# Kernel optimization log

Measured on AMD Instinct MI355X. Metric: run time of the kernel, lower is better.

The kernel has to match this reference:

```python
import jax, jax.numpy as jnp
import numpy as np

M, B, T, C, H, HS = 2, 8, 1024, 512, 8, 64
EPS = 1e-5

NAMES = ['x','sa_kw1','sa_kb1','sa_kw2','sa_qw1','sa_qb1','sa_qw2','sa_vw1','sa_vb1','sa_vw2',
         'sa_pw1','sa_pb1','sa_pw2','sa_pb2','ff_w1','ff_b1','ff_w2','ff_b2',
         'ln1_g','ln1_b','ln2_g','ln2_b','lnc_g','lnc_b',
         'ca_qw','ca_kvw','ca_pw1','ca_pb1','ca_pw2','ca_pb2']


def setup_inputs() -> dict:
    key = jax.random.key(0)
    it = iter(jax.random.split(key, 40))
    def w(shape, s=0.02):
        return jax.random.normal(next(it), shape, jnp.float32) * s
    d = {}
    d['x'] = jax.random.normal(next(it), (M, B, T, C), jnp.float32)
    # self-attention heads: Linear(C,HS//2)+bias -> tanh -> Linear(HS//2,HS) no bias, stacked over (M,H)
    for nm in ('k', 'q', 'v'):
        d['sa_%sw1' % nm] = w((M, H, C, HS // 2))
        d['sa_%sb1' % nm] = jnp.zeros((M, H, HS // 2), jnp.float32)
        d['sa_%sw2' % nm] = w((M, H, HS // 2, HS))
    # MHA output proj: Linear(H*HS,C//2)->tanh->Linear(C//2,C)
    d['sa_pw1'] = w((M, H * HS, C // 2)); d['sa_pb1'] = jnp.zeros((M, C // 2), jnp.float32)
    d['sa_pw2'] = w((M, C // 2, C));      d['sa_pb2'] = jnp.zeros((M, C), jnp.float32)
    # feed-forward
    d['ff_w1'] = w((M, C, 4 * C)); d['ff_b1'] = jnp.zeros((M, 4 * C), jnp.float32)
    d['ff_w2'] = w((M, 4 * C, C)); d['ff_b2'] = jnp.zeros((M, C), jnp.float32)
    # layernorms
    for nm in ('ln1', 'ln2', 'lnc'):
        d[nm + '_g'] = jnp.ones((M, C), jnp.float32)
        d[nm + '_b'] = jnp.zeros((M, C), jnp.float32)
    # cross-attention: per head q proj (no bias), per-kv-modality kv proj (no bias, 2*HS)
    d['ca_qw'] = w((M, H, C, HS))
    d['ca_kvw'] = w((M, H, M - 1, C, 2 * HS))
    d['ca_pw1'] = w((M, H * HS, C // 2)); d['ca_pb1'] = jnp.zeros((M, C // 2), jnp.float32)
    d['ca_pw2'] = w((M, C // 2, C));      d['ca_pb2'] = jnp.zeros((M, C), jnp.float32)
    return d


def _ln(x, g, b):
    mu = x.mean(-1, keepdims=True)
    var = ((x - mu) ** 2).mean(-1, keepdims=True)
    return (x - mu) * jax.lax.rsqrt(var + EPS) * g + b


def _attend(q, k, v, mask):
    # q,k,v: (B,H,T,HS); causal masked softmax attention
    aff = jnp.einsum('bhtd,bhsd->bhts', q, k) * (HS ** -0.5)
    aff = jnp.where(mask, aff, -jnp.inf)
    return jnp.einsum('bhts,bhsd->bhtd', jax.nn.softmax(aff, axis=-1), v)


def _merge(o):
    # (B,H,T,HS) -> (B,T,H*HS), matching torch.cat over heads
    return o.transpose(0, 2, 1, 3).reshape(o.shape[0], o.shape[2], -1)


def _forward(p):
    mask = jnp.tril(jnp.ones((T, T), bool))
    x = p['x']
    attended = []
    for i in range(M):  # fixed small modality loop
        xi = x[i]
        h = _ln(xi, p['ln1_g'][i], p['ln1_b'][i])
        def hm(w1, b1, w2):
            # batched over heads: Linear->tanh->Linear
            z = jnp.tanh(jnp.einsum('btc,hce->bhte', h, w1) + b1[:, None, :])
            return jnp.einsum('bhte,hed->bhtd', z, w2)
        o = _attend(hm(p['sa_qw1'][i], p['sa_qb1'][i], p['sa_qw2'][i]),
                    hm(p['sa_kw1'][i], p['sa_kb1'][i], p['sa_kw2'][i]),
                    hm(p['sa_vw1'][i], p['sa_vb1'][i], p['sa_vw2'][i]), mask)
        o = jnp.tanh(_merge(o) @ p['sa_pw1'][i] + p['sa_pb1'][i]) @ p['sa_pw2'][i] + p['sa_pb2'][i]
        xi = xi + o
        h2 = _ln(xi, p['ln2_g'][i], p['ln2_b'][i])
        xi = xi + (jax.nn.relu(h2 @ p['ff_w1'][i] + p['ff_b1'][i]) @ p['ff_w2'][i] + p['ff_b2'][i])
        attended.append(xi)
    outs = []
    for i in range(M):
        xi = attended[i]
        hq = _ln(xi, p['lnc_g'][i], p['lnc_b'][i])
        q = jnp.einsum('btc,hcd->bhtd', hq, p['ca_qw'][i])
        acc = 0.0
        for jidx, j in enumerate([j for j in range(M) if j != i]):
            kv = jnp.einsum('btc,hcd->bhtd', attended[j], p['ca_kvw'][i][:, jidx])
            k, v = jnp.split(kv, 2, axis=-1)
            acc = acc + _attend(q, k, v, mask)
        o = jnp.tanh(_merge(acc) @ p['ca_pw1'][i] + p['ca_pb1'][i]) @ p['ca_pw2'][i] + p['ca_pb2'][i]
        outs.append(xi + o)
    return jnp.stack(outs)


def reference(x, sa_kw1, sa_kb1, sa_kw2, sa_qw1, sa_qb1, sa_qw2, sa_vw1, sa_vb1, sa_vw2,
              sa_pw1, sa_pb1, sa_pw2, sa_pb2, ff_w1, ff_b1, ff_w2, ff_b2,
              ln1_g, ln1_b, ln2_g, ln2_b, lnc_g, lnc_b,
              ca_qw, ca_kvw, ca_pw1, ca_pb1, ca_pw2, ca_pb2):
    args = (x, sa_kw1, sa_kb1, sa_kw2, sa_qw1, sa_qb1, sa_qw2, sa_vw1, sa_vb1, sa_vw2,
            sa_pw1, sa_pb1, sa_pw2, sa_pb2, ff_w1, ff_b1, ff_w2, ff_b2,
            ln1_g, ln1_b, ln2_g, ln2_b, lnc_g, lnc_b,
            ca_qw, ca_kvw, ca_pw1, ca_pb1, ca_pw2, ca_pb2)
    return _forward(dict(zip(NAMES, args)))
```

## Files before the change

### kernel.cpp

```cpp
#include <hip/hip_runtime.h>
#include <hip/hip_bf16.h>

#define DEVI __device__ __forceinline__

typedef __attribute__((ext_vector_type(8))) short short8v;
typedef __attribute__((ext_vector_type(4))) float float4v;
typedef __attribute__((ext_vector_type(16))) float f32x16;

#if defined(__has_builtin)
#if __has_builtin(__builtin_amdgcn_exp2f)
#define EXP2F(x) __builtin_amdgcn_exp2f(x)
#endif
#endif
#ifndef EXP2F
#define EXP2F(x) exp2f(x)
#endif

constexpr int Mm = 2, Bb = 8, Tt = 1024, Cc = 512, Hh = 8, HSs = 64;
constexpr int ROWS = Bb * Tt;
constexpr size_t BTC = (size_t)Bb * Tt * Cc;
constexpr size_t SLAB = (size_t)ROWS * 512;
constexpr size_t KOFF = (size_t)2 * ROWS * 768;
constexpr size_t VOFF = KOFF + 2 * SLAB;
constexpr float SCQ = 0.18033688011112042f;

DEVI short f2bf(float f) {
    __hip_bfloat16 h = __float2bfloat16(f);
    short s; __builtin_memcpy(&s, &h, 2); return s;
}

DEVI float4v mfma16(short8v a, short8v b, float4v c) {
    return __builtin_amdgcn_mfma_f32_16x16x32_bf16(a, b, c, 0, 0, 0);
}
DEVI f32x16 mfma32(short8v a, short8v b, f32x16 c) {
    return __builtin_amdgcn_mfma_f32_32x32x16_bf16(a, b, c, 0, 0, 0);
}

DEVI void gload_lds16(const short* g, short* l) {
    __builtin_amdgcn_global_load_lds(
        (const __attribute__((address_space(1))) void*)g,
        (__attribute__((address_space(3))) void*)l, 16, 0, 0);
}

__global__ __launch_bounds__(256) void transpose_cvt(const float* __restrict__ src,
                                                     short* __restrict__ dst,
                                                     int K, int N, size_t moff, size_t hoff) {
    __shared__ float t[32][33];
    int k0 = blockIdx.x * 32, n0 = blockIdx.y * 32;
    int z = blockIdx.z;
    size_t so = (size_t)z * K * N;
    short* d = dst + (size_t)(z >> 3) * moff + (size_t)(z & 7) * hoff;
    int tx = threadIdx.x, ty = threadIdx.y;
#pragma unroll
    for (int i = 0; i < 32; i += 8)
        t[ty + i][tx] = src[so + (size_t)(k0 + ty + i) * N + n0 + tx];
    __syncthreads();
#pragma unroll
    for (int i = 0; i < 32; i += 8)
        d[(size_t)(n0 + ty + i) * K + k0 + tx] = f2bf(t[tx][ty + i]);
}

__global__ __launch_bounds__(256) void bias_cat3(const float* __restrict__ q,
                                                 const float* __restrict__ k,
                                                 const float* __restrict__ v,
                                                 float* __restrict__ o) {
    int m = blockIdx.x, t = threadIdx.x;
    o[m * 768 + t]       = q[m * 256 + t];
    o[m * 768 + 256 + t] = k[m * 256 + t];
    o[m * 768 + 512 + t] = v[m * 256 + t];
}

__global__ __launch_bounds__(256) void vtrans(const short* __restrict__ V,
                                              short* __restrict__ VT,
                                              int vrs, int hs, long long vzs) {
    __shared__ short t[32][33];
    int t0 = blockIdx.x * 32, d0 = blockIdx.y * 32;
    int z = blockIdx.z, mod = z >> 6, bh = z & 63, b = bh >> 3, h = bh & 7;
    const short* src = V + (long long)mod * vzs + (size_t)b * Tt * vrs + h * hs;
    short* dst = VT + (size_t)z * 65536;
    int tx = threadIdx.x, ty = threadIdx.y;
#pragma unroll
    for (int i = 0; i < 32; i += 8)
        t[ty + i][tx] = src[(size_t)(t0 + ty + i) * vrs + d0 + tx];
    __syncthreads();
#pragma unroll
    for (int i = 0; i < 32; i += 8)
        dst[(size_t)(d0 + ty + i) * Tt + t0 + tx] = t[tx][ty + i];
}

__global__ __launch_bounds__(256) void ln_kernel(const float* __restrict__ x,
                                                 const float* __restrict__ g,
                                                 const float* __restrict__ b,
                                                 short* __restrict__ out, size_t xzs) {
    __shared__ float ssum[4], ssq[4];
    int z = blockIdx.y;
    x += z * xzs; g += z * Cc; b += z * Cc; out += z * SLAB;
    int row = blockIdx.x, tid = threadIdx.x;
    const float* xr = x + (size_t)row * Cc;
    float v0 = xr[tid], v1 = xr[tid + 256];
    float s = v0 + v1, q = v0 * v0 + v1 * v1;
#pragma unroll
    for (int o = 1; o < 64; o <<= 1) { s += __shfl_xor(s, o, 64); q += __shfl_xor(q, o, 64); }
    int w = tid >> 6;
    if ((tid & 63) == 0) { ssum[w] = s; ssq[w] = q; }
    __syncthreads();
    s = ssum[0] + ssum[1] + ssum[2] + ssum[3];
    q = ssq[0] + ssq[1] + ssq[2] + ssq[3];
    float mu = s * (1.f / Cc);
    float var = q * (1.f / Cc) - mu * mu;
    float rs = rsqrtf(var + 1e-5f);
    short* orow = out + (size_t)row * Cc;
    orow[tid]       = f2bf((v0 - mu) * rs * g[tid]       + b[tid]);
    orow[tid + 256] = f2bf((v1 - mu) * rs * g[tid + 256] + b[tid + 256]);
}

template<int BM, int BN, int ACT, bool BIAS, bool RES, bool WF, bool WB>
__global__ __launch_bounds__(256, 2) void gemm2(
    const short* __restrict__ A, int lda, long long a_zs,
    const short* __restrict__ Wt, int ldw, long long w_zs,
    const float* __restrict__ bias, long long bias_zs,
    const float* __restrict__ res, long long res_zs,
    float* __restrict__ outF, long long outF_zs,
    short* __restrict__ outB, long long outB_zs,
    int ldc, int K, float oscale) {
    constexpr int BK = 64;
    __shared__ short As[BM][BK];
    __shared__ short Bs[BN][BK];
    long long z = blockIdx.z;
    A += z * a_zs; Wt += z * w_zs;
    if (BIAS) bias += z * bias_zs;
    if (RES)  res  += z * res_zs;
    if (WF)   outF += z * outF_zs;
    if (WB)   outB += z * outB_zs;
    int m0 = blockIdx.x * BM, n0 = blockIdx.y * BN;
    int tid = threadIdx.x, wv = tid >> 6, l = tid & 63, lr = l & 15, lg = l >> 4;
    constexpr int WM = BM / 2, WN = BN / 2;
    int wm = wv & 1, wn = wv >> 1;
    constexpr int AI = WM / 16, BJ = WN / 16;
    float4v acc[AI][BJ] = {};
    int lrow = l >> 3;
    int gcol = (l & 7) ^ lrow;
    constexpr int CHA = BM / 8, CHB = BN / 8;
    for (int k0 = 0; k0 < K; k0 += BK) {
        __syncthreads();
#pragma unroll
        for (int c = 0; c < CHA / 4; c++) {
            int ch = wv + c * 4;
            gload_lds16(&A[(size_t)(m0 + ch * 8 + lrow) * lda + k0 + gcol * 8],
                        &As[ch * 8][0]);
        }
#pragma unroll
        for (int c = 0; c < CHB / 4; c++) {
            int ch = wv + c * 4;
            gload_lds16(&Wt[(size_t)(n0 + ch * 8 + lrow) * ldw + k0 + gcol * 8],
                        &Bs[ch * 8][0]);
        }
        __syncthreads();
#pragma unroll
        for (int kk = 0; kk < 2; kk++) {
            int g = (kk * 4 + lg) ^ (lr & 7);
            short8v af[AI], bfv[BJ];
#pragma unroll
            for (int i = 0; i < AI; i++)
                af[i] = *(const short8v*)&As[wm * WM + i * 16 + lr][g * 8];
#pragma unroll
            for (int j = 0; j < BJ; j++)
                bfv[j] = *(const short8v*)&Bs[wn * WN + j * 16 + lr][g * 8];
#pragma unroll
            for (int i = 0; i < AI; i++)
#pragma unroll
                for (int j = 0; j < BJ; j++)
                    acc[i][j] = mfma16(af[i], bfv[j], acc[i][j]);
        }
    }
#pragma unroll
    for (int i = 0; i < AI; i++) {
#pragma unroll
        for (int j = 0; j < BJ; j++) {
            int col = n0 + wn * WN + j * 16 + lr;
            float bv = BIAS ? bias[col] : 0.f;
#pragma unroll
            for (int r = 0; r < 4; r++) {
                int row = m0 + wm * WM + i * 16 + lg * 4 + r;
                float v = acc[i][j][r] * oscale + bv;
                if (ACT == 1) v = tanhf(v);
                if (ACT == 2) v = fmaxf(v, 0.f);
                size_t idx = (size_t)row * ldc + col;
                if (RES) v += res[idx];
                if (WF) outF[idx] = v;
                if (WB) outB[idx] = f2bf(v);
            }
        }
    }
}

__global__ __launch_bounds__(256) void proj2(const short* __restrict__ Z,
                                             const short* __restrict__ W2,
                                             short* __restrict__ Qo,
                                             short* __restrict__ Ko,
                                             short* __restrict__ VTo,
                                             float qscale) {
    __shared__ short As[64][40], Ws[64][40];
    __shared__ short Tv[64][72];
    int zz = blockIdx.y, t = zz >> 4, m = (zz >> 3) & 1, h = zz & 7;
    int m0 = blockIdx.x * 64;
    const short* Ap = Z + (size_t)m * ((size_t)ROWS * 768) + t * 256 + h * 32;
    const short* Wp = W2 + (size_t)zz * 2048;
    float sc = (t == 0) ? qscale : 1.0f;
    int tid = threadIdx.x, w = tid >> 6, l = tid & 63, lr = l & 15, lg = l >> 4;
    int r = tid >> 2, c = (tid & 3) * 8;
    *(short8v*)&As[r][c] = *(const short8v*)&Ap[(size_t)(m0 + r) * 768 + c];
    *(short8v*)&Ws[r][c] = *(const short8v*)&Wp[r * 32 + c];
    __syncthreads();
    short8v af = *(const short8v*)&As[w * 16 + lr][lg * 8];
    float4v acc[4] = {};
#pragma unroll
    for (int j = 0; j < 4; j++) {
        short8v bf = *(const short8v*)&Ws[j * 16 + lr][lg * 8];
        acc[j] = mfma16(af, bf, acc[j]);
    }
    if (t < 2) {
        short* Op = (t == 0 ? Qo : Ko) + (size_t)m * SLAB + h * 64;
#pragma unroll
        for (int j = 0; j < 4; j++)
#pragma unroll
            for (int rr = 0; rr < 4; rr++)
                Op[(size_t)(m0 + w * 16 + lg * 4 + rr) * 512 + j * 16 + lr] =
                    f2bf(acc[j][rr] * sc);
    } else {
#pragma unroll
        for (int j = 0; j < 4; j++)
#pragma unroll
            for (int rr = 0; rr < 4; rr++)
                Tv[j * 16 + lr][w * 16 + lg * 4 + rr] = f2bf(acc[j][rr]);
        __syncthreads();
        int b = m0 >> 10, trow0 = m0 & 1023;
        int z64 = m * 64 + b * 8 + h;
        short* dst = VTo + (size_t)z64 * 65536;
        int d = w * 16 + (l >> 2), toff = (l & 3) * 16;
        *(short8v*)&dst[(size_t)d * Tt + trow0 + toff]     = *(const short8v*)&Tv[d][toff];
        *(short8v*)&dst[(size_t)d * Tt + trow0 + toff + 8] = *(const short8v*)&Tv[d][toff + 8];
    }
}

__global__ __launch_bounds__(512, 4) void flash_attn4(
    const short* __restrict__ Q, const short* __restrict__ K,
    const short* __restrict__ VT, short* __restrict__ O,
    int krs, int khs, long long qzs, long long kzs, long long vtzs, long long ozs)
{
    __shared__ short Ks[2][64][64];
    __shared__ short Vs[2][64][64];
    int id = blockIdx.x;
    int bh = id & 63, mod = (id >> 6) & 1, p = (id >> 7) & 3;
    Q += (long long)mod * qzs; K += (long long)mod * kzs;
    VT += (long long)mod * vtzs; O += (long long)mod * ozs;
    int b = bh >> 3, h = bh & 7;
    int tid = threadIdx.x, w = tid >> 6, l = tid & 63;
    int lq = l & 31, hi = l >> 5;
    int strip = (w < 4) ? p : 7 - p;
    int qwb = strip * 128 + (w & 3) * 32;
    int qabs = qwb + lq;
    const short* Qp = Q + (size_t)b * Tt * Cc + h * HSs;
    const short* Kp = K + (size_t)b * Tt * krs + h * khs;
    const short* Vp = VT + (size_t)bh * HSs * Tt;
    short* Op = O + (size_t)b * Tt * Cc + h * HSs;

    short8v qf[4];
#pragma unroll
    for (int c = 0; c < 4; c++)
        qf[c] = *(const short8v*)&Qp[(size_t)qabs * Cc + (c * 2 + hi) * 8];

    f32x16 oacc[2] = {};
    float mrun = -1e30f, lrun = 0.f;
    int nk = 2 * (7 - p) + 2;
    short8v pk, pv;

    auto LOADT = [&](int kb) {
        int r = tid >> 3, cg = (tid & 7) ^ (r & 7);
        pk = *(const short8v*)&Kp[(size_t)(kb + r) * krs + cg * 8];
        pv = *(const short8v*)&Vp[(size_t)r * Tt + kb + cg * 8];
    };
    auto STORET = [&](int bi) {
        int r = tid >> 3, cp = tid & 7;
        *(short8v*)&Ks[bi][r][cp * 8] = pk;
        *(short8v*)&Vs[bi][r][cp * 8] = pv;
    };

    LOADT(0); STORET(0); __syncthreads();

    for (int t = 0; t < nk; t++) {
        int cur = t & 1, kb = t * 64;
        bool pre = (t + 1 < nk);
        if (pre) LOADT(kb + 64);
        if (kb <= qwb + 31) {
            bool full = (kb + 63 <= qwb);
            f32x16 st[2] = {};
            __builtin_amdgcn_s_setprio(1);
#pragma unroll
            for (int kh = 0; kh < 2; kh++) {
#pragma unroll
                for (int cc = 0; cc < 4; cc++) {
                    int r = kh * 32 + lq;
                    int cp = (cc * 2 + hi) ^ (r & 7);
                    short8v af = *(const short8v*)&Ks[cur][r][cp * 8];
                    st[kh] = mfma32(af, qf[cc], st[kh]);
                }
            }
            __builtin_amdgcn_s_setprio(0);
            float pr[32];
            if (full) {
#pragma unroll
                for (int kh = 0; kh < 2; kh++)
#pragma unroll
                    for (int r = 0; r < 16; r++) pr[kh * 16 + r] = st[kh][r];
            } else {
#pragma unroll
                for (int kh = 0; kh < 2; kh++)
#pragma unroll
                    for (int r = 0; r < 16; r++) {
                        int kabs = kb + kh * 32 + (r & 3) + 8 * (r >> 2) + 4 * hi;
                        pr[kh * 16 + r] = (kabs <= qabs) ? st[kh][r] : -3.0e38f;
                    }
            }
            float t16[16];
#pragma unroll
            for (int i = 0; i < 16; i++) t16[i] = fmaxf(pr[i], pr[i + 16]);
#pragma unroll
            for (int i = 0; i < 8; i++) t16[i] = fmaxf(t16[i], t16[i + 8]);
            float mx = fmaxf(fmaxf(fmaxf(t16[0], t16[4]), fmaxf(t16[1], t16[5])),
                             fmaxf(fmaxf(t16[2], t16[6]), fmaxf(t16[3], t16[7])));
            mx = fmaxf(mx, __shfl_xor(mx, 32));
            if (!__all(mx <= mrun + 11.5f)) {
                float mn = fmaxf(mrun, mx);
                float al = EXP2F(mrun - mn);
                mrun = mn;
                lrun *= al;
#pragma unroll
                for (int dh = 0; dh < 2; dh++)
#pragma unroll
                    for (int r = 0; r < 16; r++) oacc[dh][r] *= al;
            }
#pragma unroll
            for (int i = 0; i < 32; i++) pr[i] = EXP2F(pr[i] - mrun);
            float s16[16];
#pragma unroll
            for (int i = 0; i < 16; i++) s16[i] = pr[i] + pr[i + 16];
#pragma unroll
            for (int i = 0; i < 8; i++) s16[i] = s16[i] + s16[i + 8];
            float rsum = ((s16[0] + s16[4]) + (s16[1] + s16[5])) +
                         ((s16[2] + s16[6]) + (s16[3] + s16[7]));
            rsum += __shfl_xor(rsum, 32);
            lrun += rsum;
#pragma unroll
            for (int ks = 0; ks < 4; ks++) {
                unsigned x0, x1, y0, y1;
                asm("v_cvt_pk_bf16_f32 %0, %1, %2" : "=v"(x0) : "v"(pr[ks*8+0]), "v"(pr[ks*8+1]));
                asm("v_cvt_pk_bf16_f32 %0, %1, %2" : "=v"(x1) : "v"(pr[ks*8+2]), "v"(pr[ks*8+3]));
                asm("v_cvt_pk_bf16_f32 %0, %1, %2" : "=v"(y0) : "v"(pr[ks*8+4]), "v"(pr[ks*8+5]));
                asm("v_cvt_pk_bf16_f32 %0, %1, %2" : "=v"(y1) : "v"(pr[ks*8+6]), "v"(pr[ks*8+7]));
                asm volatile("v_permlane32_swap_b32 %0, %1" : "+v"(x0), "+v"(y0));
                asm volatile("v_permlane32_swap_b32 %0, %1" : "+v"(x1), "+v"(y1));
                union { unsigned u[4]; short8v s; } uu;
                uu.u[0] = x0; uu.u[1] = x1; uu.u[2] = y0; uu.u[3] = y1;
                __builtin_amdgcn_s_setprio(1);
#pragma unroll
                for (int dh = 0; dh < 2; dh++) {
                    int r = dh * 32 + lq;
                    int cp = (ks * 2 + hi) ^ (r & 7);
                    short8v vf = *(const short8v*)&Vs[cur][r][cp * 8];
                    oacc[dh] = mfma32(vf, uu.s, oacc[dh]);
                }
                __builtin_amdgcn_s_setprio(0);
            }
        }
        if (pre) STORET(cur ^ 1);
        __syncthreads();
    }
    float inv = 1.f / lrun;
#pragma unroll
    for (int dh = 0; dh < 2; dh++)
#pragma unroll
        for (int r = 0; r < 16; r += 2) {
            unsigned wds;
            float a0 = oacc[dh][r] * inv, a1 = oacc[dh][r + 1] * inv;
            asm("v_cvt_pk_bf16_f32 %0, %1, %2" : "=v"(wds) : "v"(a0), "v"(a1));
            int d = (r & 3) + 8 * (r >> 2) + 4 * hi + dh * 32;
            *(unsigned*)&Op[(size_t)qabs * Cc + d] = wds;
        }
}

extern "C" void kernel_launch(void* const* d_in, const int* in_sizes, int n_in,
                              void* d_out, int out_size, void* d_ws, size_t ws_size,
                              hipStream_t stream) {
    (void)in_sizes; (void)n_in; (void)out_size; (void)ws_size;
    const float* X     = (const float*)d_in[0];
    const float* saKW1 = (const float*)d_in[1];
    const float* saKB1 = (const float*)d_in[2];
    const float* saKW2 = (const float*)d_in[3];
    const float* saQW1 = (const float*)d_in[4];
    const float* saQB1 = (const float*)d_in[5];
    const float* saQW2 = (const float*)d_in[6];
    const float* saVW1 = (const float*)d_in[7];
    const float* saVB1 = (const float*)d_in[8];
    const float* saVW2 = (const float*)d_in[9];
    const float* saPW1 = (const float*)d_in[10];
    const float* saPB1 = (const float*)d_in[11];
    const float* saPW2 = (const float*)d_in[12];
    const float* saPB2 = (const float*)d_in[13];
    const float* ffW1  = (const float*)d_in[14];
    const float* ffB1  = (const float*)d_in[15];
    const float* ffW2  = (const float*)d_in[16];
    const float* ffB2  = (const float*)d_in[17];
    const float* ln1g  = (const float*)d_in[18];
    const float* ln1b  = (const float*)d_in[19];
    const float* ln2g  = (const float*)d_in[20];
    const float* ln2b  = (const float*)d_in[21];
    const float* lncg  = (const float*)d_in[22];
    const float* lncb  = (const float*)d_in[23];
    const float* caQW  = (const float*)d_in[24];
    const float* caKVW = (const float*)d_in[25];
    const float* caPW1 = (const float*)d_in[26];
    const float* caPB1 = (const float*)d_in[27];
    const float* caPW2 = (const float*)d_in[28];
    const float* caPB2 = (const float*)d_in[29];
    float* OUT = (float*)d_out;

    char* ws = (char*)d_ws;
    size_t cur = 0;
    auto alloc = [&](size_t bytes) -> char* {
        char* p = ws + cur; cur += (bytes + 255) & ~(size_t)255; return p;
    };

    short* WT = (short*)alloc((size_t)7700480 * 2);
    size_t wo = 0;
    auto wslot = [&](size_t e) -> short* { short* p = WT + wo; wo += e; return p; };
    short* w_qkv1 = wslot(786432);
    short* w_qkv2 = wslot(98304);
    short* w_pw1 = wslot(262144); short* w_pw2 = wslot(262144);
    short* w_ff1 = wslot(2097152); short* w_ff2 = wslot(2097152);
    short* w_caq = wslot(524288);  short* w_cakv = wslot(1048576);
    short* w_cp1 = wslot(262144);  short* w_cp2 = wslot(262144);
    float* bqkv = (float*)alloc(2 * 768 * 4);

    short* Hb  = (short*)alloc(2 * SLAB * 2);
    short* Qb  = (short*)alloc(2 * SLAB * 2);
    short* Obf = (short*)alloc(2 * SLAB * 2);
    short* Fb  = (short*)alloc((size_t)2 * ROWS * 2048 * 2);
    short* AB  = (short*)alloc(2 * SLAB * 2);
    short* VTb = Hb;
    short* P1b = Hb;
    short* Kb = Fb + KOFF;

    dim3 tb32(32, 8, 1);
    auto TC = [&](const float* s, short* d, int K, int N, int slices, size_t moff, size_t hoff) {
        transpose_cvt<<<dim3(K / 32, N / 32, slices), tb32, 0, stream>>>(s, d, K, N, moff, hoff);
    };
    TC(saQW1, w_qkv1,          512, 32, 16, 393216, 16384);
    TC(saKW1, w_qkv1 + 131072, 512, 32, 16, 393216, 16384);
    TC(saVW1, w_qkv1 + 262144, 512, 32, 16, 393216, 16384);
    TC(saQW2, w_qkv2,          32, 64, 16, 16384, 2048);
    TC(saKW2, w_qkv2 + 32768,  32, 64, 16, 16384, 2048);
    TC(saVW2, w_qkv2 + 65536,  32, 64, 16, 16384, 2048);
    TC(saPW1, w_pw1, 512, 256, 2, 0, 131072);
    TC(saPW2, w_pw2, 256, 512, 2, 0, 131072);
    TC(ffW1,  w_ff1, 512, 2048, 2, 0, 1048576);
    TC(ffW2,  w_ff2, 2048, 512, 2, 0, 1048576);
    TC(caQW,  w_caq, 512, 64, 16, 262144, 32768);
    TC(caKVW, w_cakv, 512, 128, 16, 524288, 65536);
    TC(caPW1, w_cp1, 512, 256, 2, 0, 131072);
    TC(caPW2, w_cp2, 256, 512, 2, 0, 131072);
    bias_cat3<<<2, 256, 0, stream>>>(saQB1, saKB1, saVB1, bqkv);

    ln_kernel<<<dim3(ROWS, 2), 256, 0, stream>>>(X, ln1g, ln1b, Hb, BTC);
    gemm2<128, 128, 1, true, false, false, true><<<dim3(64, 6, 2), 256, 0, stream>>>(
        Hb, 512, SLAB, w_qkv1, 512, 393216, bqkv, 768,
        nullptr, 0, nullptr, 0, Fb, (long long)ROWS * 768, 768, 512, 1.0f);
    proj2<<<dim3(128, 48), 256, 0, stream>>>(Fb, w_qkv2, Qb, Kb, VTb, SCQ);
    flash_attn4<<<dim3(512), 512, 0, stream>>>(
        Qb, Kb, VTb, Obf, 512, 64, SLAB, SLAB, 4194304, SLAB);
    gemm2<64, 128, 1, true, false, false, true><<<dim3(128, 2, 2), 256, 0, stream>>>(
        Obf, 512, SLAB, w_pw1, 512, 131072, saPB1, 256,
        nullptr, 0, nullptr, 0, P1b, (long long)ROWS * 256, 256, 512, 1.0f);
    gemm2<64, 128, 0, true, true, true, false><<<dim3(128, 4, 2), 256, 0, stream>>>(
        P1b, 256, (long long)ROWS * 256, w_pw2, 256, 131072, saPB2, 512,
        X, BTC, OUT, BTC, nullptr, 0, 512, 256, 1.0f);
    ln_kernel<<<dim3(ROWS, 2), 256, 0, stream>>>(OUT, ln2g, ln2b, Hb, BTC);
    gemm2<128, 128, 2, true, false, false, true><<<dim3(64, 16, 2), 256, 0, stream>>>(
        Hb, 512, SLAB, w_ff1, 512, 1048576, ffB1, 2048,
        nullptr, 0, nullptr, 0, Fb, (long long)ROWS * 2048, 2048, 512, 1.0f);
    gemm2<64, 128, 0, true, true, true, true><<<dim3(128, 4, 2), 256, 0, stream>>>(
        Fb, 2048, (long long)ROWS * 2048, w_ff2, 2048, 1048576, ffB2, 512,
        OUT, BTC, OUT, BTC, AB, SLAB, 512, 2048, 1.0f);

    ln_kernel<<<dim3(ROWS, 2), 256, 0, stream>>>(OUT, lncg, lncb, Hb, BTC);
    gemm2<64, 128, 0, false, false, false, true><<<dim3(128, 4, 2), 256, 0, stream>>>(
        Hb, 512, SLAB, w_caq, 512, 262144, nullptr, 0,
        nullptr, 0, nullptr, 0, Qb, SLAB, 512, 512, SCQ);
    gemm2<128, 128, 0, false, false, false, true><<<dim3(64, 8, 2), 256, 0, stream>>>(
        AB + SLAB, 512, -(long long)SLAB, w_cakv, 512, 524288, nullptr, 0,
        nullptr, 0, nullptr, 0, Fb, (long long)ROWS * 1024, 1024, 512, 1.0f);
    vtrans<<<dim3(32, 2, 128), tb32, 0, stream>>>(Fb + 64, VTb, 1024, 128, (long long)ROWS * 1024);
    flash_attn4<<<dim3(512), 512, 0, stream>>>(
        Qb, Fb, VTb, Obf, 1024, 128, SLAB, (long long)ROWS * 1024, 4194304, SLAB);
    gemm2<64, 128, 1, true, false, false, true><<<dim3(128, 2, 2), 256, 0, stream>>>(
        Obf, 512, SLAB, w_cp1, 512, 131072, caPB1, 256,
        nullptr, 0, nullptr, 0, P1b, (long long)ROWS * 256, 256, 512, 1.0f);
    gemm2<64, 128, 0, true, true, true, false><<<dim3(128, 4, 2), 256, 0, stream>>>(
        P1b, 256, (long long)ROWS * 256, w_cp2, 256, 131072, caPB2, 512,
        OUT, BTC, OUT, BTC, nullptr, 0, 512, 256, 1.0f);
}
```

Before: 397.1 us.

## Add double-buffered 128x128 GEMM kernel and use it for most projections

Measured after the change: 407.5 us. 1.03x slower.

```diff
diff --git a/kernel.cpp b/kernel.cpp
--- a/kernel.cpp
+++ b/kernel.cpp
@@ -112,6 +112,94 @@
     short* orow = out + (size_t)row * Cc;
     orow[tid]       = f2bf((v0 - mu) * rs * g[tid]       + b[tid]);
     orow[tid + 256] = f2bf((v1 - mu) * rs * g[tid + 256] + b[tid + 256]);
+}
+
+template<int ACT, bool BIAS, bool RES, bool WF, bool WB>
+__global__ __launch_bounds__(256, 2) void gemm3(
+    const short* __restrict__ A, int lda, long long a_zs,
+    const short* __restrict__ Wt, int ldw, long long w_zs,
+    const float* __restrict__ bias, long long bias_zs,
+    const float* __restrict__ res, long long res_zs,
+    float* __restrict__ outF, long long outF_zs,
+    short* __restrict__ outB, long long outB_zs,
+    int ldc, int K, float oscale) {
+    constexpr int BM = 128, BN = 128, BK = 64;
+    __shared__ short As[2][BM][BK];
+    __shared__ short Bs[2][BN][BK];
+    long long z = blockIdx.z;
+    A += z * a_zs; Wt += z * w_zs;
+    if (BIAS) bias += z * bias_zs;
+    if (RES)  res  += z * res_zs;
+    if (WF)   outF += z * outF_zs;
+    if (WB)   outB += z * outB_zs;
+    int m0 = blockIdx.x * BM, n0 = blockIdx.y * BN;
+    int tid = threadIdx.x, wv = tid >> 6, l = tid & 63;
+    int lq = l & 31, hi = l >> 5;
+    int wm = wv & 1, wn = wv >> 1;
+    f32x16 acc[2][2] = {};
+    int lrow = l >> 3;
+    int gcol = (l & 7) ^ lrow;
+
+    auto STAGE = [&](int bi, int k0) {
+#pragma unroll
+        for (int c = 0; c < 4; c++) {
+            int ch = wv + c * 4;
+            gload_lds16(&A[(size_t)(m0 + ch * 8 + lrow) * lda + k0 + gcol * 8],
+                        &As[bi][ch * 8][0]);
+        }
+#pragma unroll
+        for (int c = 0; c < 4; c++) {
+            int ch = wv + c * 4;
+            gload_lds16(&Wt[(size_t)(n0 + ch * 8 + lrow) * ldw + k0 + gcol * 8],
+                        &Bs[bi][ch * 8][0]);
+        }
+    };
+
+    STAGE(0, 0);
+    __syncthreads();
+    int NT = K / BK;
+    for (int t = 0; t < NT; t++) {
+        int cur = t & 1;
+        if (t + 1 < NT) STAGE(cur ^ 1, (t + 1) * BK);
+        const short (*Ac)[BK] = As[cur];
+        const short (*Bc)[BK] = Bs[cur];
+#pragma unroll
+        for (int ks = 0; ks < 4; ks++) {
+            int g = (ks * 2 + hi) ^ (lq & 7);
+            short8v af[2], bf[2];
+#pragma unroll
+            for (int i = 0; i < 2; i++)
+                af[i] = *(const short8v*)&Ac[wm * 64 + i * 32 + lq][g * 8];
+#pragma unroll
+            for (int j = 0; j < 2; j++)
+                bf[j] = *(const short8v*)&Bc[wn * 64 + j * 32 + lq][g * 8];
+#pragma unroll
+            for (int i = 0; i < 2; i++)
+#pragma unroll
+                for (int j = 0; j < 2; j++)
+                    acc[i][j] = mfma32(af[i], bf[j], acc[i][j]);
+        }
+        __syncthreads();
+    }
+#pragma unroll
+    for (int i = 0; i < 2; i++) {
+#pragma unroll
+        for (int j = 0; j < 2; j++) {
+            int col = n0 + wn * 64 + j * 32 + lq;
+            float bv = BIAS ? bias[col] : 0.f;
+#pragma unroll
+            for (int r = 0; r < 16; r++) {
+                int row = m0 + wm * 64 + i * 32 + 4 * hi + (r & 3) + 8 * (r >> 2);
+                float v = acc[i][j][r] * oscale + bv;
+                if (ACT == 1) v = tanhf(v);
+                if (ACT == 2) v = fmaxf(v, 0.f);
+                size_t idx = (size_t)row * ldc + col;
+                if (RES) v += res[idx];
+                if (WF) outF[idx] = v;
+                if (WB) outB[idx] = f2bf(v);
+            }
+        }
+    }
 }
 
 template<int BM, int BN, int ACT, bool BIAS, bool RES, bool WF, bool WB>
@@ -472,7 +560,7 @@
     bias_cat3<<<2, 256, 0, stream>>>(saQB1, saKB1, saVB1, bqkv);
 
     ln_kernel<<<dim3(ROWS, 2), 256, 0, stream>>>(X, ln1g, ln1b, Hb, BTC);
-    gemm2<128, 128, 1, true, false, false, true><<<dim3(64, 6, 2), 256, 0, stream>>>(
+    gemm3<1, true, false, false, true><<<dim3(64, 6, 2), 256, 0, stream>>>(
         Hb, 512, SLAB, w_qkv1, 512, 393216, bqkv, 768,
         nullptr, 0, nullptr, 0, Fb, (long long)ROWS * 768, 768, 512, 1.0f);
     proj2<<<dim3(128, 48), 256, 0, stream>>>(Fb, w_qkv2, Qb, Kb, VTb, SCQ);
@@ -481,22 +569,22 @@
     gemm2<64, 128, 1, true, false, false, true><<<dim3(128, 2, 2), 256, 0, stream>>>(
         Obf, 512, SLAB, w_pw1, 512, 131072, saPB1, 256,
         nullptr, 0, nullptr, 0, P1b, (long long)ROWS * 256, 256, 512, 1.0f);
-    gemm2<64, 128, 0, true, true, true, false><<<dim3(128, 4, 2), 256, 0, stream>>>(
+    gemm3<0, true, true, true, false><<<dim3(64, 4, 2), 256, 0, stream>>>(
         P1b, 256, (long long)ROWS * 256, w_pw2, 256, 131072, saPB2, 512,
         X, BTC, OUT, BTC, nullptr, 0, 512, 256, 1.0f);
     ln_kernel<<<dim3(ROWS, 2), 256, 0, stream>>>(OUT, ln2g, ln2b, Hb, BTC);
-    gemm2<128, 128, 2, true, false, false, true><<<dim3(64, 16, 2), 256, 0, stream>>>(
+    gemm3<2, true, false, false, true><<<dim3(64, 16, 2), 256, 0, stream>>>(
         Hb, 512, SLAB, w_ff1, 512, 1048576, ffB1, 2048,
         nullptr, 0, nullptr, 0, Fb, (long long)ROWS * 2048, 2048, 512, 1.0f);
-    gemm2<64, 128, 0, true, true, true, true><<<dim3(128, 4, 2), 256, 0, stream>>>(
+    gemm3<0, true, true, true, true><<<dim3(64, 4, 2), 256, 0, stream>>>(
         Fb, 2048, (long long)ROWS * 2048, w_ff2, 2048, 1048576, ffB2, 512,
         OUT, BTC, OUT, BTC, AB, SLAB, 512, 2048, 1.0f);
 
     ln_kernel<<<dim3(ROWS, 2), 256, 0, stream>>>(OUT, lncg, lncb, Hb, BTC);
-    gemm2<64, 128, 0, false, false, false, true><<<dim3(128, 4, 2), 256, 0, stream>>>(
+    gemm3<0, false, false, false, true><<<dim3(64, 4, 2), 256, 0, stream>>>(
         Hb, 512, SLAB, w_caq, 512, 262144, nullptr, 0,
         nullptr, 0, nullptr, 0, Qb, SLAB, 512, 512, SCQ);
-    gemm2<128, 128, 0, false, false, false, true><<<dim3(64, 8, 2), 256, 0, stream>>>(
+    gemm3<0, false, false, false, true><<<dim3(64, 8, 2), 256, 0, stream>>>(
         AB + SLAB, 512, -(long long)SLAB, w_cakv, 512, 524288, nullptr, 0,
         nullptr, 0, nullptr, 0, Fb, (long long)ROWS * 1024, 1024, 512, 1.0f);
     vtrans<<<dim3(32, 2, 128), tb32, 0, stream>>>(Fb + 64, VTb, 1024, 128, (long long)ROWS * 1024);
@@ -505,7 +593,7 @@
     gemm2<64, 128, 1, true, false, false, true><<<dim3(128, 2, 2), 256, 0, stream>>>(
         Obf, 512, SLAB, w_cp1, 512, 131072, caPB1, 256,
         nullptr, 0, nullptr, 0, P1b, (long long)ROWS * 256, 256, 512, 1.0f);
-    gemm2<64, 128, 0, true, true, true, false><<<dim3(128, 4, 2), 256, 0, stream>>>(
+    gemm3<0, true, true, true, false><<<dim3(64, 4, 2), 256, 0, stream>>>(
         P1b, 256, (long long)ROWS * 256, w_cp2, 256, 131072, caPB2, 512,
         OUT, BTC, OUT, BTC, nullptr, 0, 512, 256, 1.0f);
 }
```
